# Optimization experiments

Measured on AMD Instinct MI355X. Metric: run time of the kernel, lower is better.

The kernel has to match this reference:

```python
import jax, jax.numpy as jnp
import numpy as np

B, C, S, H, W = 8, 64, 64, 128, 128
HID = 32           # max(C//2, 8)
STEPS, DT, OMEGA_MAX = 10, 0.3, 2.0
EPS = 1e-5


def _dw(x, k):
    # depthwise 3x3 conv, NCHW, kernel [C,1,3,3]
    return jax.lax.conv_general_dilated(
        x, k, (1, 1), 'SAME',
        dimension_numbers=('NCHW', 'OIHW', 'NCHW'),
        feature_group_count=x.shape[1])


def _pw(x, w, b=None):
    # pointwise (1x1) conv as einsum, w: [out,in]
    y = jnp.einsum('bihw,oi->bohw', x, w)
    return y if b is None else y + b[None, :, None, None]


def _lrelu(x):
    return jax.nn.leaky_relu(x, 0.2)


def setup_inputs() -> dict:
    key = jax.random.key(0)
    ks = jax.random.split(key, 16)
    d = {
        'force': jax.random.normal(ks[0], (B, C, H, W), jnp.float32),
        'style': jax.random.normal(ks[1], (1, S, 1, 1), jnp.float32),
        'illum_feat': jax.random.normal(ks[2], (B, C, H, W), jnp.float32),
        # HyperEncoder 1x1 convs
        'h_w1': 0.05 * jax.random.normal(ks[3], (HID, C + S), jnp.float32),
        'h_b1': jnp.zeros((HID,), jnp.float32),
        'h_w2': 0.05 * jax.random.normal(ks[4], (HID, HID), jnp.float32),
        'h_b2': jnp.zeros((HID,), jnp.float32),
        'h_w3': 0.05 * jax.random.normal(ks[5], (4 * C, HID), jnp.float32),
        'h_b3': jnp.zeros((4 * C,), jnp.float32),
        # OscillatorCell convs (no bias)
        'dw_k': 0.05 * jax.random.normal(ks[6], (C, 1, 3, 3), jnp.float32),
        'pw_w': 0.05 * jax.random.normal(ks[7], (C, C), jnp.float32),
        # refine: dw3x3 (+bias), pw, lrelu, pw
        'r_dw_k': 0.05 * jax.random.normal(ks[8], (C, 1, 3, 3), jnp.float32),
        'r_dw_b': jnp.zeros((C,), jnp.float32),
        'r_pw1_w': 0.05 * jax.random.normal(ks[9], (C, C), jnp.float32),
        'r_pw1_b': jnp.zeros((C,), jnp.float32),
        'r_pw2_w': 0.05 * jax.random.normal(ks[10], (C, C), jnp.float32),
        'r_pw2_b': jnp.zeros((C,), jnp.float32),
        'layer_scale': 0.01 * jnp.ones((1, C, 1, 1), jnp.float32),
    }
    return d


def reference(force, style, illum_feat,
              h_w1, h_b1, h_w2, h_b2, h_w3, h_b3,
              dw_k, pw_w,
              r_dw_k, r_dw_b, r_pw1_w, r_pw1_b, r_pw2_w, r_pw2_b,
              layer_scale):
    force = force + 0.2 * illum_feat
    b, c, h, w = force.shape

    # HyperEncoder
    style_map = jnp.broadcast_to(style, (b, style.shape[1], h, w))
    u = jnp.concatenate([force, style_map], axis=1)
    u = _lrelu(_pw(u, h_w1, h_b1))
    u = _lrelu(_pw(u, h_w2, h_b2))
    p = _pw(u, h_w3, h_b3)
    wch, zch, gch, bch = jnp.split(p, 4, axis=1)
    omega = jax.nn.sigmoid(wch) * OMEGA_MAX
    zeta = jax.nn.sigmoid(zch)
    gamma = jax.nn.sigmoid(gch) * 2.0
    beta = jnp.tanh(bch)

    # unrolled symplectic-Euler oscillator recurrence
    def step(carry, _):
        x, v = carry
        coupling = _dw(x, dw_k) + _pw(x, pw_w)
        accel = force + coupling - 2.0 * zeta * omega * v - omega ** 2 * x
        v = v + accel * DT
        x = x + v * DT
        return (x, v), None

    x0 = jnp.zeros_like(force)
    (x, v), _ = jax.lax.scan(step, (x0, x0), None, length=STEPS)

    # instance norm (no affine) + style modulation
    fx = force + x
    mu = fx.mean(axis=(2, 3), keepdims=True)
    var = fx.var(axis=(2, 3), keepdims=True)
    out = gamma * ((fx - mu) / jnp.sqrt(var + EPS)) + beta

    # refine branch with layer scale
    r = _dw(out, r_dw_k) + r_dw_b[None, :, None, None]
    r = _lrelu(_pw(r, r_pw1_w, r_pw1_b))
    r = _pw(r, r_pw2_w, r_pw2_b)
    out = out + layer_scale * r
    return (out, x, v)
```

## Files before the change

kernel.cpp:

```cpp
#include <hip/hip_runtime.h>
#include <hip/hip_fp16.h>

#define Hn 128
#define Wn 128
#define HWn 16384
#define Cn 64
#define Bn 8
#define NTOT (Bn*Cn*HWn)
#define NPIX (Bn*HWn)
#define DTc 0.3f
#define EPSc 1e-5f

__device__ __forceinline__ float sigm(float t){ return 1.0f/(1.0f+__expf(-t)); }

__global__ void fuseF0(const float4* __restrict__ force, const float4* __restrict__ illum,
                       __half* __restrict__ F, __half* __restrict__ XA, __half* __restrict__ V)
{
    int i = blockIdx.x * blockDim.x + threadIdx.x;
    float4 f = force[i], il = illum[i];
    float a0 = f.x + 0.2f*il.x, a1 = f.y + 0.2f*il.y;
    float a2 = f.z + 0.2f*il.z, a3 = f.w + 0.2f*il.w;
    uint2 pf, px, pv;
    __half2 h;
    h = __floats2half2_rn(a0, a1);            pf.x = *(unsigned int*)&h;
    h = __floats2half2_rn(a2, a3);            pf.y = *(unsigned int*)&h;
    h = __floats2half2_rn(0.09f*a0, 0.09f*a1); px.x = *(unsigned int*)&h;
    h = __floats2half2_rn(0.09f*a2, 0.09f*a3); px.y = *(unsigned int*)&h;
    h = __floats2half2_rn(0.3f*a0, 0.3f*a1);   pv.x = *(unsigned int*)&h;
    h = __floats2half2_rn(0.3f*a2, 0.3f*a3);   pv.y = *(unsigned int*)&h;
    *reinterpret_cast<uint2*>(F  + 4*(size_t)i) = pf;
    *reinterpret_cast<uint2*>(XA + 4*(size_t)i) = px;
    *reinterpret_cast<uint2*>(V  + 4*(size_t)i) = pv;
}

__global__ void prep(const float* __restrict__ style, const float* __restrict__ w1,
                     const float* __restrict__ b1, const float* __restrict__ pw,
                     const float* __restrict__ pw1, const float* __restrict__ pw2,
                     const float* __restrict__ w3, const float* __restrict__ b3,
                     float* __restrict__ w1T, float* __restrict__ c1,
                     float* __restrict__ pwT, float* __restrict__ pw1T,
                     float* __restrict__ pw2T,
                     __half2* __restrict__ w3abP, __half2* __restrict__ w3gbP,
                     __half2* __restrict__ b3abP, __half2* __restrict__ b3gbP)
{
    int t = threadIdx.x;
    if (t < 32) {
        float s = b1[t];
        for (int k = 0; k < 64; k++) s += w1[t*128 + 64 + k] * style[k];
        c1[t] = s;
    }
    for (int i = t; i < 2048; i += 256) { int c = i >> 5, j = i & 31; w1T[i] = w1[j*128 + c]; }
    for (int i = t; i < 4096; i += 256) {
        int c = i >> 6, k = i & 63;
        pwT[i]  = pw[k*64 + c];
        pw1T[i] = pw1[k*64 + c];
        pw2T[i] = pw2[k*64 + c];
    }
    for (int i = t; i < 2048; i += 256) {
        int j = i >> 5, k = i & 31;
        w3abP[i] = __floats2half2_rn(w3[j*32 + k],         w3[(64 + j)*32 + k]);
        w3gbP[i] = __floats2half2_rn(w3[(128 + j)*32 + k], w3[(192 + j)*32 + k]);
    }
    if (t < 64) {
        b3abP[t] = __floats2half2_rn(b3[t],       b3[64 + t]);
        b3gbP[t] = __floats2half2_rn(b3[128 + t], b3[192 + t]);
    }
}

__global__ void hyperM(const __half* __restrict__ F,
                       const float* __restrict__ w1T, const float* __restrict__ c1,
                       const float* __restrict__ w2, const float* __restrict__ b2,
                       const __half2* __restrict__ w3abP, const __half2* __restrict__ w3gbP,
                       const __half2* __restrict__ b3abP, const __half2* __restrict__ b3gbP,
                       __half2* __restrict__ AB, __half2* __restrict__ GB)
{
    int p = blockIdx.x * blockDim.x + threadIdx.x;
    int b  = p >> 14;
    int sp = p & (HWn - 1);
    int base = b * Cn * HWn + sp;

    float u1[32];
#pragma unroll
    for (int j = 0; j < 32; j++) u1[j] = c1[j];
#pragma unroll 4
    for (int c = 0; c < 64; c++) {
        float fc = __half2float(F[base + c*HWn]);
        const float* __restrict__ wr = w1T + c*32;
#pragma unroll
        for (int j = 0; j < 32; j++) u1[j] += wr[j] * fc;
    }
#pragma unroll
    for (int j = 0; j < 32; j++) { float v = u1[j]; u1[j] = v > 0.f ? v : 0.2f*v; }

    float u2[32];
#pragma unroll
    for (int i = 0; i < 32; i++) {
        float s = b2[i];
#pragma unroll
        for (int j = 0; j < 32; j++) s += w2[i*32 + j] * u1[j];
        u2[i] = s > 0.f ? s : 0.2f*s;
    }
    __half2 u2b[32];
#pragma unroll
    for (int i = 0; i < 32; i++) u2b[i] = __half2half2(__float2half(u2[i]));

#pragma unroll 2
    for (int j = 0; j < 64; j++) {
        __half2 aab = b3abP[j];
        __half2 agb = b3gbP[j];
        const __half2* __restrict__ wa = w3abP + j*32;
        const __half2* __restrict__ wg = w3gbP + j*32;
#pragma unroll
        for (int i = 0; i < 32; i++) {
            aab = __hfma2(wa[i], u2b[i], aab);
            agb = __hfma2(wg[i], u2b[i], agb);
        }
        float2 tab = __half22float2(aab);
        float om = 2.0f * sigm(tab.x);
        float ze = sigm(tab.y);
        AB[base + j*HWn] = __floats2half2_rn(2.0f * ze * om, om * om);
        float2 tgb = __half22float2(agb);
        GB[base + j*HWn] = __floats2half2_rn(2.0f * sigm(tgb.x), tanhf(tgb.y));
    }
}

template <bool LAST>
__global__ void osc_step(const __half* __restrict__ Xin, __half* __restrict__ Xout,
                         __half* __restrict__ V, const __half* __restrict__ F,
                         const __half2* __restrict__ AB,
                         const float* __restrict__ dwk, const float* __restrict__ pwT,
                         float* __restrict__ Xf, float* __restrict__ Vf)
{
    int wid  = blockIdx.x;
    int slot = wid >> 3;
    int pc   = ((wid & 7) << 6) + (slot >> 2);
    int c0   = (slot & 3) << 4;
    int p = (pc << 8) + threadIdx.x;
    int b  = p >> 14;
    int sp = p & (HWn - 1);
    int y = sp >> 7, x = sp & 127;
    int base = b * Cn * HWn + sp;

    float acc[16];
#pragma unroll
    for (int k = 0; k < 16; k++) acc[k] = 0.f;
#pragma unroll 4
    for (int c = 0; c < 64; c++) {
        float xc = __half2float(Xin[base + c*HWn]);
        const float* __restrict__ wr = pwT + c*64 + c0;
#pragma unroll
        for (int k = 0; k < 16; k++) acc[k] += wr[k] * xc;
    }

    int   yo[3] = { y > 0 ? -Wn : 0, 0, y < Hn-1 ? Wn : 0 };
    int   xo[3] = { x > 0 ? -1  : 0, 0, x < Wn-1 ? 1  : 0 };
    float my[3] = { y > 0 ? 1.f : 0.f, 1.f, y < Hn-1 ? 1.f : 0.f };
    float mx[3] = { x > 0 ? 1.f : 0.f, 1.f, x < Wn-1 ? 1.f : 0.f };
    float mm[9]; int oo[9];
#pragma unroll
    for (int dy = 0; dy < 3; dy++)
#pragma unroll
        for (int dx = 0; dx < 3; dx++) { mm[dy*3+dx] = my[dy]*mx[dx]; oo[dy*3+dx] = yo[dy]+xo[dx]; }

#pragma unroll
    for (int cc = 0; cc < 16; cc++) {
        int c = c0 + cc;
        int cb = base + c*HWn;
        float tv[9];
#pragma unroll
        for (int t = 0; t < 9; t++) tv[t] = __half2float(Xin[cb + oo[t]]);
        float dws = 0.f;
#pragma unroll
        for (int t = 0; t < 9; t++) dws += (dwk[c*9 + t] * mm[t]) * tv[t];
        float xc = tv[4];
        float2 ab = __half22float2(AB[cb]);
        float vv = __half2float(V[cb]);
        float accel = __half2float(F[cb]) + acc[cc] + dws - ab.x * vv - ab.y * xc;
        vv += accel * DTc;
        float xn = xc + vv * DTc;
        if constexpr (!LAST) {
            V[cb] = __float2half(vv);
            Xout[cb] = __float2half(xn);
        } else {
            Xf[cb] = xn;
            Vf[cb] = vv;
        }
    }
}

__global__ void inorm_stats(const __half* __restrict__ F, const float* __restrict__ X,
                            float* __restrict__ mu, float* __restrict__ rs)
{
    int bc = blockIdx.x;
    int base = bc * HWn;
    const __half2* __restrict__ F2 = (const __half2*)(F + base);
    const float4*  __restrict__ X4 = (const float4*)(X + base);
    float s = 0.f, s2 = 0.f;
    for (int i = threadIdx.x; i < HWn/4; i += blockDim.x) {
        float4 xv = X4[i];
        float2 f0 = __half22float2(F2[2*i]);
        float2 f1 = __half22float2(F2[2*i+1]);
        float v0 = f0.x + xv.x, v1 = f0.y + xv.y, v2 = f1.x + xv.z, v3 = f1.y + xv.w;
        s += (v0 + v1) + (v2 + v3);
        s2 += (v0*v0 + v1*v1) + (v2*v2 + v3*v3);
    }
#pragma unroll
    for (int o = 32; o > 0; o >>= 1) { s += __shfl_down(s, o); s2 += __shfl_down(s2, o); }
    __shared__ float sh[16];
    int w = threadIdx.x >> 6, l = threadIdx.x & 63;
    if (l == 0) { sh[w] = s; sh[8 + w] = s2; }
    __syncthreads();
    if (threadIdx.x == 0) {
        float S = 0.f, S2 = 0.f;
        for (int i = 0; i < 4; i++) { S += sh[i]; S2 += sh[8 + i]; }
        float m = S / (float)HWn;
        float var = S2 / (float)HWn - m*m;
        mu[bc] = m;
        rs[bc] = rsqrtf(var + EPSc);
    }
}

__global__ void modulate(const __half* __restrict__ F, const float4* __restrict__ X4,
                         const uint4* __restrict__ GBu, const float* __restrict__ mu,
                         const float* __restrict__ rs, __half* __restrict__ outp)
{
    int e4 = blockIdx.x * blockDim.x + threadIdx.x;
    int bc = e4 >> 12;
    float m = mu[bc], r = rs[bc];
    uint2 fu = *reinterpret_cast<const uint2*>(F + 4*(size_t)e4);
    float2 f0 = __half22float2(*(__half2*)&fu.x);
    float2 f1 = __half22float2(*(__half2*)&fu.y);
    float4 xv = X4[e4];
    uint4 gb = GBu[e4];
    float2 g0 = __half22float2(*(__half2*)&gb.x);
    float2 g1 = __half22float2(*(__half2*)&gb.y);
    float2 g2 = __half22float2(*(__half2*)&gb.z);
    float2 g3 = __half22float2(*(__half2*)&gb.w);
    float o0 = g0.x * ((f0.x + xv.x - m) * r) + g0.y;
    float o1 = g1.x * ((f0.y + xv.y - m) * r) + g1.y;
    float o2 = g2.x * ((f1.x + xv.z - m) * r) + g2.y;
    float o3 = g3.x * ((f1.y + xv.w - m) * r) + g3.y;
    __half2 h01 = __floats2half2_rn(o0, o1);
    __half2 h23 = __floats2half2_rn(o2, o3);
    uint2 pack; pack.x = *(unsigned int*)&h01; pack.y = *(unsigned int*)&h23;
    *reinterpret_cast<uint2*>(outp + 4*(size_t)e4) = pack;
}

__global__ __launch_bounds__(512)
void refine(const __half* __restrict__ outp,
            const float* __restrict__ rdwk, const float* __restrict__ rdwb,
            const float* __restrict__ pw1T, const float* __restrict__ pb1,
            const float* __restrict__ pw2T, const float* __restrict__ pb2,
            const float* __restrict__ ls, float* __restrict__ out)
{
    __shared__ unsigned int rv2_s[64][64];
    __shared__ unsigned int act2_s[64][64];
    __shared__ __half w1s[64][64];
    __shared__ __half w2s[64][64];
    __shared__ float  dwks[576];
    __shared__ __half2 pb1h[32], pb2h[32];
    __shared__ float  rdwbs[64], lss[64];
    int t = threadIdx.x;
    for (int i = t; i < 4096; i += 512) {
        w1s[i>>6][i&63] = __float2half(pw1T[i]);
        w2s[i>>6][i&63] = __float2half(pw2T[i]);
    }
    for (int i = t; i < 576; i += 512) dwks[i] = rdwk[i];
    if (t < 64) { rdwbs[t]=rdwb[t]; lss[t]=ls[t]; }
    if (t < 32) {
        pb1h[t] = __floats2half2_rn(pb1[2*t], pb1[2*t+1]);
        pb2h[t] = __floats2half2_rn(pb2[2*t], pb2[2*t+1]);
    }

    int l  = t & 63;
    int g  = t >> 6;
    int c0 = g << 3;
    int row = blockIdx.x;
    int b = row >> 7, y = row & 127;
    int base = b * Cn * HWn + y * Wn;
    int px0 = l << 1;

    int   yo[3] = { y > 0 ? -Wn : 0, 0, y < Hn-1 ? Wn : 0 };
    float my[3] = { y > 0 ? 1.f : 0.f, 1.f, y < Hn-1 ? 1.f : 0.f };
    float wl = l > 0  ? 1.f : 0.f;
    float wr = l < 63 ? 1.f : 0.f;
    int loff = l > 0 ? -1 : 0;
    __syncthreads();

#pragma unroll
    for (int cc = 0; cc < 8; cc++) {
        int c = c0 + cc;
        int cb = base + c*HWn + px0;
        float rv0 = rdwbs[c], rv1 = rdwbs[c];
#pragma unroll
        for (int r = 0; r < 3; r++) {
            const __half* __restrict__ rp = outp + cb + yo[r];
            unsigned int cu = *reinterpret_cast<const unsigned int*>(rp);
            float2 ct = __half22float2(*(__half2*)&cu);
            float lf = __half2float(rp[loff]);
            float rt = __half2float(rp[2]);
            float k0 = dwks[c*9 + r*3 + 0] * my[r];
            float k1 = dwks[c*9 + r*3 + 1] * my[r];
            float k2 = dwks[c*9 + r*3 + 2] * my[r];
            rv0 += k0*(wl*lf) + k1*ct.x + k2*ct.y;
            rv1 += k0*ct.x + k1*ct.y + k2*(wr*rt);
        }
        __half2 hv = __floats2half2_rn(rv0, rv1);
        rv2_s[c][l] = *(unsigned int*)&hv;
    }
    __syncthreads();

    __half2 accA[4], accB[4];
#pragma unroll
    for (int q = 0; q < 4; q++) { accA[q] = pb1h[(c0 >> 1) + q]; accB[q] = accA[q]; }
#pragma unroll 8
    for (int c = 0; c < 64; c++) {
        unsigned int rvu = rv2_s[c][l];
        __half2 rvp = *(__half2*)&rvu;
        __half2 r0 = __half2half2(__low2half(rvp));
        __half2 r1 = __half2half2(__high2half(rvp));
        uint4 wq = *reinterpret_cast<const uint4*>(&w1s[c][c0]);
        __half2 w01 = *(__half2*)&wq.x, w23 = *(__half2*)&wq.y;
        __half2 w45 = *(__half2*)&wq.z, w67 = *(__half2*)&wq.w;
        accA[0] = __hfma2(w01, r0, accA[0]); accB[0] = __hfma2(w01, r1, accB[0]);
        accA[1] = __hfma2(w23, r0, accA[1]); accB[1] = __hfma2(w23, r1, accB[1]);
        accA[2] = __hfma2(w45, r0, accA[2]); accB[2] = __hfma2(w45, r1, accB[2]);
        accA[3] = __hfma2(w67, r0, accA[3]); accB[3] = __hfma2(w67, r1, accB[3]);
    }
#pragma unroll
    for (int q = 0; q < 4; q++) {
        float2 a0 = __half22float2(accA[q]);
        float2 a1 = __half22float2(accB[q]);
        float e0 = a0.x > 0.f ? a0.x : 0.2f*a0.x;
        float e1 = a0.y > 0.f ? a0.y : 0.2f*a0.y;
        float e2 = a1.x > 0.f ? a1.x : 0.2f*a1.x;
        float e3 = a1.y > 0.f ? a1.y : 0.2f*a1.y;
        __half2 p0 = __floats2half2_rn(e0, e2);
        __half2 p1 = __floats2half2_rn(e1, e3);
        act2_s[c0 + 2*q][l]     = *(unsigned int*)&p0;
        act2_s[c0 + 2*q + 1][l] = *(unsigned int*)&p1;
    }
    __syncthreads();

#pragma unroll
    for (int q = 0; q < 4; q++) { accA[q] = pb2h[(c0 >> 1) + q]; accB[q] = accA[q]; }
#pragma unroll 8
    for (int j = 0; j < 64; j++) {
        unsigned int au = act2_s[j][l];
        __half2 ap = *(__half2*)&au;
        __half2 a0 = __half2half2(__low2half(ap));
        __half2 a1 = __half2half2(__high2half(ap));
        uint4 wq = *reinterpret_cast<const uint4*>(&w2s[j][c0]);
        __half2 w01 = *(__half2*)&wq.x, w23 = *(__half2*)&wq.y;
        __half2 w45 = *(__half2*)&wq.z, w67 = *(__half2*)&wq.w;
        accA[0] = __hfma2(w01, a0, accA[0]); accB[0] = __hfma2(w01, a1, accB[0]);
        accA[1] = __hfma2(w23, a0, accA[1]); accB[1] = __hfma2(w23, a1, accB[1]);
        accA[2] = __hfma2(w45, a0, accA[2]); accB[2] = __hfma2(w45, a1, accB[2]);
        accA[3] = __hfma2(w67, a0, accA[3]); accB[3] = __hfma2(w67, a1, accB[3]);
    }
#pragma unroll
    for (int q = 0; q < 4; q++) {
        float2 a0 = __half22float2(accA[q]);
        float2 a1 = __half22float2(accB[q]);
        int ca = c0 + 2*q, cb2 = ca + 1;
        int ba = base + ca*HWn + px0;
        int bb = base + cb2*HWn + px0;
        unsigned int oua = *reinterpret_cast<const unsigned int*>(outp + ba);
        unsigned int oub = *reinterpret_cast<const unsigned int*>(outp + bb);
        float2 oa = __half22float2(*(__half2*)&oua);
        float2 ob = __half22float2(*(__half2*)&oub);
        float la = lss[ca], lb = lss[cb2];
        *reinterpret_cast<float2*>(out + ba) = make_float2(oa.x + la*a0.x, oa.y + la*a1.x);
        *reinterpret_cast<float2*>(out + bb) = make_float2(ob.x + lb*a0.y, ob.y + lb*a1.y);
    }
}

extern "C" void kernel_launch(void* const* d_in, const int* in_sizes, int n_in,
                              void* d_out, int out_size, void* d_ws, size_t ws_size,
                              hipStream_t stream)
{
    (void)in_sizes; (void)n_in; (void)out_size; (void)ws_size;
    const float* force   = (const float*)d_in[0];
    const float* style   = (const float*)d_in[1];
    const float* illum   = (const float*)d_in[2];
    const float* h_w1    = (const float*)d_in[3];
    const float* h_b1    = (const float*)d_in[4];
    const float* h_w2    = (const float*)d_in[5];
    const float* h_b2    = (const float*)d_in[6];
    const float* h_w3    = (const float*)d_in[7];
    const float* h_b3    = (const float*)d_in[8];
    const float* dw_k    = (const float*)d_in[9];
    const float* pw_w    = (const float*)d_in[10];
    const float* r_dw_k  = (const float*)d_in[11];
    const float* r_dw_b  = (const float*)d_in[12];
    const float* r_pw1_w = (const float*)d_in[13];
    const float* r_pw1_b = (const float*)d_in[14];
    const float* r_pw2_w = (const float*)d_in[15];
    const float* r_pw2_b = (const float*)d_in[16];
    const float* lscale  = (const float*)d_in[17];

    float* out  = (float*)d_out;
    float* Xf32 = out + (size_t)NTOT;
    float* Vf32 = out + 2*(size_t)NTOT;
    __half2* GB = (__half2*)out;

    char* w = (char*)d_ws;
    __half2* AB = (__half2*)w; w += (size_t)NTOT*4;
    __half*  F  = (__half*)w;  w += (size_t)NTOT*2;
    __half*  XA = (__half*)w;  w += (size_t)NTOT*2;
    __half*  XB = (__half*)w;  w += (size_t)NTOT*2;
    __half*  Vh = (__half*)w;  w += (size_t)NTOT*2;
    float* w1T  = (float*)w;
    float* c1   = w1T + 2048;
    float* pwT  = c1 + 32;
    float* pw1T = pwT + 4096;
    float* pw2T = pw1T + 4096;
    float* mu   = pw2T + 4096;
    float* rs   = mu + 512;
    __half2* w3abP = (__half2*)(rs + 512);
    __half2* w3gbP = w3abP + 2048;
    __half2* b3abP = w3gbP + 2048;
    __half2* b3gbP = b3abP + 64;
    __half* outp = (__half*)AB;

    fuseF0<<<NTOT/1024, 256, 0, stream>>>((const float4*)force, (const float4*)illum,
                                          F, XA, Vh);
    prep<<<1, 256, 0, stream>>>(style, h_w1, h_b1, pw_w, r_pw1_w, r_pw2_w, h_w3, h_b3,
                                w1T, c1, pwT, pw1T, pw2T, w3abP, w3gbP, b3abP, b3gbP);
    hyperM<<<NPIX/256, 256, 0, stream>>>(F, w1T, c1, h_w2, h_b2,
                                         w3abP, w3gbP, b3abP, b3gbP, AB, GB);
    for (int s = 1; s <= 8; s++) {
        const __half* xin = (s & 1) ? XA : XB;
        __half*      xout = (s & 1) ? XB : XA;
        osc_step<false><<<2048, 256, 0, stream>>>(xin, xout, Vh, F, AB,
                                                  dw_k, pwT, nullptr, nullptr);
    }
    osc_step<true><<<2048, 256, 0, stream>>>(XA, XB, Vh, F, AB,
                                             dw_k, pwT, Xf32, Vf32);
    inorm_stats<<<Bn*Cn, 256, 0, stream>>>(F, Xf32, mu, rs);
    modulate<<<NTOT/1024, 256, 0, stream>>>(F, (const float4*)Xf32,
                                            (const uint4*)GB, mu, rs, outp);
    refine<<<NPIX/128, 512, 0, stream>>>(outp, r_dw_k, r_dw_b, pw1T, r_pw1_b,
                                         pw2T, r_pw2_b, lscale, out);
}
```

Measured before the change: 495.1 us.

## Stage oscillator stencil and hyper inputs in LDS, split hyper output heads

Each osc_step block now handles one half-row across all 64 channels. It stages the three input rows plus halo in shared memory, so the pointwise and 3x3 depthwise reads come from LDS instead of repeated global gathers. The hyper encoder loads its F tile into shared memory with vector loads. It also splits the AB and GB output heads across a second grid dimension, which adds parallelism but recomputes the first two layers twice. The trade-off is extra LDS traffic, a block-level sync, and duplicated hyper MLP work.

After: 911.9 us. +84.2%, slower.

```diff
diff --git a/kernel.cpp b/kernel.cpp
--- a/kernel.cpp
+++ b/kernel.cpp
@@ -67,24 +67,38 @@
     }
 }
 
-__global__ void hyperM(const __half* __restrict__ F,
-                       const float* __restrict__ w1T, const float* __restrict__ c1,
-                       const float* __restrict__ w2, const float* __restrict__ b2,
-                       const __half2* __restrict__ w3abP, const __half2* __restrict__ w3gbP,
-                       const __half2* __restrict__ b3abP, const __half2* __restrict__ b3gbP,
-                       __half2* __restrict__ AB, __half2* __restrict__ GB)
-{
-    int p = blockIdx.x * blockDim.x + threadIdx.x;
-    int b  = p >> 14;
-    int sp = p & (HWn - 1);
-    int base = b * Cn * HWn + sp;
+__global__ __launch_bounds__(256)
+void hyperS(const __half* __restrict__ F,
+            const float* __restrict__ w1T, const float* __restrict__ c1,
+            const float* __restrict__ w2, const float* __restrict__ b2,
+            const __half2* __restrict__ w3abP, const __half2* __restrict__ w3gbP,
+            const __half2* __restrict__ b3abP, const __half2* __restrict__ b3gbP,
+            __half2* __restrict__ AB, __half2* __restrict__ GB)
+{
+    __shared__ __half fs[64][256];
+    int t = threadIdx.x;
+    int p0 = blockIdx.x << 8;
+    int b  = p0 >> 14;
+    int sp0 = p0 & (HWn - 1);
+    int tbase = b * Cn * HWn + sp0;
+
+#pragma unroll
+    for (int it = 0; it < 8; it++) {
+        int f = t + (it << 8);
+        int c = f >> 5, u = f & 31;
+        uint4 d = *reinterpret_cast<const uint4*>(F + tbase + c*HWn + (u << 3));
+        *reinterpret_cast<uint4*>(&fs[c][u << 3]) = d;
+    }
+    __syncthreads();
+
+    int base = tbase + t;
 
     float u1[32];
 #pragma unroll
     for (int j = 0; j < 32; j++) u1[j] = c1[j];
 #pragma unroll 4
     for (int c = 0; c < 64; c++) {
-        float fc = __half2float(F[base + c*HWn]);
+        float fc = __half2float(fs[c][t]);
         const float* __restrict__ wr = w1T + c*32;
 #pragma unroll
         for (int j = 0; j < 32; j++) u1[j] += wr[j] * fc;
@@ -104,75 +118,104 @@
 #pragma unroll
     for (int i = 0; i < 32; i++) u2b[i] = __half2half2(__float2half(u2[i]));
 
+    if (blockIdx.y == 0) {
 #pragma unroll 2
-    for (int j = 0; j < 64; j++) {
-        __half2 aab = b3abP[j];
-        __half2 agb = b3gbP[j];
-        const __half2* __restrict__ wa = w3abP + j*32;
-        const __half2* __restrict__ wg = w3gbP + j*32;
-#pragma unroll
-        for (int i = 0; i < 32; i++) {
-            aab = __hfma2(wa[i], u2b[i], aab);
-            agb = __hfma2(wg[i], u2b[i], agb);
+        for (int j = 0; j < 64; j++) {
+            __half2 aab = b3abP[j];
+            const __half2* __restrict__ wa = w3abP + j*32;
+#pragma unroll
+            for (int i = 0; i < 32; i++) aab = __hfma2(wa[i], u2b[i], aab);
+            float2 tab = __half22float2(aab);
+            float om = 2.0f * sigm(tab.x);
+            float ze = sigm(tab.y);
+            AB[base + j*HWn] = __floats2half2_rn(2.0f * ze * om, om * om);
         }
-        float2 tab = __half22float2(aab);
-        float om = 2.0f * sigm(tab.x);
-        float ze = sigm(tab.y);
-        AB[base + j*HWn] = __floats2half2_rn(2.0f * ze * om, om * om);
-        float2 tgb = __half22float2(agb);
-        GB[base + j*HWn] = __floats2half2_rn(2.0f * sigm(tgb.x), tanhf(tgb.y));
+    } else {
+#pragma unroll 2
+        for (int j = 0; j < 64; j++) {
+            __half2 agb = b3gbP[j];
+            const __half2* __restrict__ wg = w3gbP + j*32;
+#pragma unroll
+            for (int i = 0; i < 32; i++) agb = __hfma2(wg[i], u2b[i], agb);
+            float2 tgb = __half22float2(agb);
+            GB[base + j*HWn] = __floats2half2_rn(2.0f * sigm(tgb.x), tanhf(tgb.y));
+        }
     }
 }
 
 template <bool LAST>
-__global__ void osc_step(const __half* __restrict__ Xin, __half* __restrict__ Xout,
-                         __half* __restrict__ V, const __half* __restrict__ F,
-                         const __half2* __restrict__ AB,
-                         const float* __restrict__ dwk, const float* __restrict__ pwT,
-                         float* __restrict__ Xf, float* __restrict__ Vf)
-{
-    int wid  = blockIdx.x;
-    int slot = wid >> 3;
-    int pc   = ((wid & 7) << 6) + (slot >> 2);
-    int c0   = (slot & 3) << 4;
-    int p = (pc << 8) + threadIdx.x;
-    int b  = p >> 14;
-    int sp = p & (HWn - 1);
-    int y = sp >> 7, x = sp & 127;
-    int base = b * Cn * HWn + sp;
+__global__ __launch_bounds__(256)
+void osc_step(const __half* __restrict__ Xin, __half* __restrict__ Xout,
+              __half* __restrict__ V, const __half* __restrict__ F,
+              const __half2* __restrict__ AB,
+              const float* __restrict__ dwk, const float* __restrict__ pwT,
+              float* __restrict__ Xf, float* __restrict__ Vf)
+{
+    __shared__ __half xs[64][3][68];
+    int wid = blockIdx.x;
+    int hp  = ((wid & 7) << 8) + (wid >> 3);
+    int b   = hp >> 8;
+    int hr  = hp & 255;
+    int y   = hr >> 1;
+    int xh  = (hr & 1) << 6;
+    int t   = threadIdx.x;
+    int base0 = b * Cn * HWn + y * Wn + xh;
+
+    int   yo[3] = { y > 0 ? -Wn : 0, 0, y < Hn-1 ? Wn : 0 };
+    float my[3] = { y > 0 ? 1.f : 0.f, 1.f, y < Hn-1 ? 1.f : 0.f };
+
+#pragma unroll
+    for (int it = 0; it < 24; it++) {
+        int f = t + (it << 8);
+        int c = f / 96;
+        int rem = f - c*96;
+        int r = rem >> 5;
+        int u = rem & 31;
+        unsigned int d = *reinterpret_cast<const unsigned int*>(Xin + base0 + c*HWn + yo[r] + (u << 1));
+        *reinterpret_cast<unsigned int*>(&xs[c][r][2 + (u << 1)]) = d;
+    }
+    for (int hv = t; hv < 384; hv += 256) {
+        int c = hv / 6;
+        int rem = hv - c*6;
+        int r = rem >> 1;
+        int side = rem & 1;
+        xs[c][r][side ? 66 : 1] = Xin[base0 + c*HWn + yo[r] + (side ? 64 : -1)];
+    }
+    __syncthreads();
+
+    int l  = t & 63;
+    int c0 = (t >> 6) << 4;
+    int x  = xh + l;
+    float wl = x > 0      ? 1.f : 0.f;
+    float wr = x < Wn - 1 ? 1.f : 0.f;
 
     float acc[16];
 #pragma unroll
     for (int k = 0; k < 16; k++) acc[k] = 0.f;
 #pragma unroll 4
     for (int c = 0; c < 64; c++) {
-        float xc = __half2float(Xin[base + c*HWn]);
-        const float* __restrict__ wr = pwT + c*64 + c0;
-#pragma unroll
-        for (int k = 0; k < 16; k++) acc[k] += wr[k] * xc;
-    }
-
-    int   yo[3] = { y > 0 ? -Wn : 0, 0, y < Hn-1 ? Wn : 0 };
-    int   xo[3] = { x > 0 ? -1  : 0, 0, x < Wn-1 ? 1  : 0 };
-    float my[3] = { y > 0 ? 1.f : 0.f, 1.f, y < Hn-1 ? 1.f : 0.f };
-    float mx[3] = { x > 0 ? 1.f : 0.f, 1.f, x < Wn-1 ? 1.f : 0.f };
-    float mm[9]; int oo[9];
-#pragma unroll
-    for (int dy = 0; dy < 3; dy++)
-#pragma unroll
-        for (int dx = 0; dx < 3; dx++) { mm[dy*3+dx] = my[dy]*mx[dx]; oo[dy*3+dx] = yo[dy]+xo[dx]; }
+        float xc = __half2float(xs[c][1][2 + l]);
+        const float* __restrict__ wrow = pwT + c*64 + c0;
+#pragma unroll
+        for (int k = 0; k < 16; k++) acc[k] += wrow[k] * xc;
+    }
 
 #pragma unroll
     for (int cc = 0; cc < 16; cc++) {
         int c = c0 + cc;
-        int cb = base + c*HWn;
-        float tv[9];
-#pragma unroll
-        for (int t = 0; t < 9; t++) tv[t] = __half2float(Xin[cb + oo[t]]);
+        int cb = base0 + l + c*HWn;
         float dws = 0.f;
 #pragma unroll
-        for (int t = 0; t < 9; t++) dws += (dwk[c*9 + t] * mm[t]) * tv[t];
-        float xc = tv[4];
+        for (int r = 0; r < 3; r++) {
+            float lf = __half2float(xs[c][r][1 + l]);
+            float ct = __half2float(xs[c][r][2 + l]);
+            float rt = __half2float(xs[c][r][3 + l]);
+            float k0 = dwk[c*9 + r*3 + 0] * my[r];
+            float k1 = dwk[c*9 + r*3 + 1] * my[r];
+            float k2 = dwk[c*9 + r*3 + 2] * my[r];
+            dws += k0 * (wl * lf) + k1 * ct + k2 * (wr * rt);
+        }
+        float xc = __half2float(xs[c][1][2 + l]);
         float2 ab = __half22float2(AB[cb]);
         float vv = __half2float(V[cb]);
         float accel = __half2float(F[cb]) + acc[cc] + dws - ab.x * vv - ab.y * xc;
@@ -427,8 +470,8 @@
                                           F, XA, Vh);
     prep<<<1, 256, 0, stream>>>(style, h_w1, h_b1, pw_w, r_pw1_w, r_pw2_w, h_w3, h_b3,
                                 w1T, c1, pwT, pw1T, pw2T, w3abP, w3gbP, b3abP, b3gbP);
-    hyperM<<<NPIX/256, 256, 0, stream>>>(F, w1T, c1, h_w2, h_b2,
-                                         w3abP, w3gbP, b3abP, b3gbP, AB, GB);
+    hyperS<<<dim3(NPIX/256, 2), 256, 0, stream>>>(F, w1T, c1, h_w2, h_b2,
+                                                  w3abP, w3gbP, b3abP, b3gbP, AB, GB);
     for (int s = 1; s <= 8; s++) {
         const __half* xin = (s & 1) ? XA : XB;
         __half*      xout = (s & 1) ? XB : XA;
```

## Split hyper-encoder into hidden-layer kernel and two-way output-head kernel

Applied to the files above, without the earlier changes.

The fused hyper-encoder kernel is split in two. The first computes the two hidden layers per pixel, staging F through shared memory with vectorized loads, and writes a 32-half hidden vector per pixel into scratch space borrowed from the X output buffer. The second reads that vector and uses a 2-wide grid in y, so the omega/zeta head and the gamma/beta head run in separate blocks. The aim is more parallelism and lower register pressure per thread, at the cost of an extra round trip through global memory for the intermediate and one more launch.

Result: faster. 482.4 us (-2.6%).

```diff
diff --git a/kernel.cpp b/kernel.cpp
--- a/kernel.cpp
+++ b/kernel.cpp
@@ -67,60 +67,109 @@
     }
 }
 
-__global__ void hyperM(const __half* __restrict__ F,
-                       const float* __restrict__ w1T, const float* __restrict__ c1,
-                       const float* __restrict__ w2, const float* __restrict__ b2,
-                       const __half2* __restrict__ w3abP, const __half2* __restrict__ w3gbP,
-                       const __half2* __restrict__ b3abP, const __half2* __restrict__ b3gbP,
-                       __half2* __restrict__ AB, __half2* __restrict__ GB)
+__global__ __launch_bounds__(256)
+void hyperU(const __half* __restrict__ F,
+            const float* __restrict__ w1T, const float* __restrict__ c1,
+            const float* __restrict__ w2, const float* __restrict__ b2,
+            __half* __restrict__ U2)
+{
+    __shared__ __half fs[64][256];
+    int t = threadIdx.x;
+    int p0 = blockIdx.x << 8;
+    int b  = p0 >> 14;
+    int sp0 = p0 & (HWn - 1);
+    int tbase = b * Cn * HWn + sp0;
+
+#pragma unroll
+    for (int it = 0; it < 8; it++) {
+        int f = t + (it << 8);
+        int c = f >> 5, u = f & 31;
+        uint4 d = *reinterpret_cast<const uint4*>(F + tbase + c*HWn + (u << 3));
+        *reinterpret_cast<uint4*>(&fs[c][u << 3]) = d;
+    }
+    __syncthreads();
+
+    float u1[32];
+#pragma unroll
+    for (int j = 0; j < 32; j++) u1[j] = c1[j];
+#pragma unroll 4
+    for (int c = 0; c < 64; c++) {
+        float fc = __half2float(fs[c][t]);
+        const float* __restrict__ wr = w1T + c*32;
+#pragma unroll
+        for (int j = 0; j < 32; j++) u1[j] += wr[j] * fc;
+    }
+#pragma unroll
+    for (int j = 0; j < 32; j++) { float v = u1[j]; u1[j] = v > 0.f ? v : 0.2f*v; }
+
+    float u2[32];
+#pragma unroll
+    for (int i = 0; i < 32; i++) {
+        float s = b2[i];
+#pragma unroll
+        for (int j = 0; j < 32; j++) s += w2[i*32 + j] * u1[j];
+        u2[i] = s > 0.f ? s : 0.2f*s;
+    }
+
+    uint4* dst = reinterpret_cast<uint4*>(U2 + ((size_t)(p0 + t)) * 32);
+#pragma unroll
+    for (int q = 0; q < 4; q++) {
+        __half2 h0 = __floats2half2_rn(u2[8*q+0], u2[8*q+1]);
+        __half2 h1 = __floats2half2_rn(u2[8*q+2], u2[8*q+3]);
+        __half2 h2 = __floats2half2_rn(u2[8*q+4], u2[8*q+5]);
+        __half2 h3 = __floats2half2_rn(u2[8*q+6], u2[8*q+7]);
+        uint4 d;
+        d.x = *(unsigned int*)&h0; d.y = *(unsigned int*)&h1;
+        d.z = *(unsigned int*)&h2; d.w = *(unsigned int*)&h3;
+        dst[q] = d;
+    }
+}
+
+__global__ __launch_bounds__(256)
+void hyperW(const __half* __restrict__ U2,
+            const __half2* __restrict__ w3abP, const __half2* __restrict__ w3gbP,
+            const __half2* __restrict__ b3abP, const __half2* __restrict__ b3gbP,
+            __half2* __restrict__ AB, __half2* __restrict__ GB)
 {
     int p = blockIdx.x * blockDim.x + threadIdx.x;
     int b  = p >> 14;
     int sp = p & (HWn - 1);
     int base = b * Cn * HWn + sp;
 
-    float u1[32];
-#pragma unroll
-    for (int j = 0; j < 32; j++) u1[j] = c1[j];
-#pragma unroll 4
-    for (int c = 0; c < 64; c++) {
-        float fc = __half2float(F[base + c*HWn]);
-        const float* __restrict__ wr = w1T + c*32;
-#pragma unroll
-        for (int j = 0; j < 32; j++) u1[j] += wr[j] * fc;
-    }
-#pragma unroll
-    for (int j = 0; j < 32; j++) { float v = u1[j]; u1[j] = v > 0.f ? v : 0.2f*v; }
-
-    float u2[32];
-#pragma unroll
-    for (int i = 0; i < 32; i++) {
-        float s = b2[i];
-#pragma unroll
-        for (int j = 0; j < 32; j++) s += w2[i*32 + j] * u1[j];
-        u2[i] = s > 0.f ? s : 0.2f*s;
-    }
     __half2 u2b[32];
-#pragma unroll
-    for (int i = 0; i < 32; i++) u2b[i] = __half2half2(__float2half(u2[i]));
-
+    const uint4* src = reinterpret_cast<const uint4*>(U2 + (size_t)p * 32);
+#pragma unroll
+    for (int q = 0; q < 4; q++) {
+        uint4 d = src[q];
+        __half2 h;
+        h = *(__half2*)&d.x; u2b[8*q+0] = __half2half2(__low2half(h)); u2b[8*q+1] = __half2half2(__high2half(h));
+        h = *(__half2*)&d.y; u2b[8*q+2] = __half2half2(__low2half(h)); u2b[8*q+3] = __half2half2(__high2half(h));
+        h = *(__half2*)&d.z; u2b[8*q+4] = __half2half2(__low2half(h)); u2b[8*q+5] = __half2half2(__high2half(h));
+        h = *(__half2*)&d.w; u2b[8*q+6] = __half2half2(__low2half(h)); u2b[8*q+7] = __half2half2(__high2half(h));
+    }
+
+    if (blockIdx.y == 0) {
 #pragma unroll 2
-    for (int j = 0; j < 64; j++) {
-        __half2 aab = b3abP[j];
-        __half2 agb = b3gbP[j];
-        const __half2* __restrict__ wa = w3abP + j*32;
-        const __half2* __restrict__ wg = w3gbP + j*32;
-#pragma unroll
-        for (int i = 0; i < 32; i++) {
-            aab = __hfma2(wa[i], u2b[i], aab);
-            agb = __hfma2(wg[i], u2b[i], agb);
+        for (int j = 0; j < 64; j++) {
+            __half2 aab = b3abP[j];
+            const __half2* __restrict__ wa = w3abP + j*32;
+#pragma unroll
+            for (int i = 0; i < 32; i++) aab = __hfma2(wa[i], u2b[i], aab);
+            float2 tab = __half22float2(aab);
+            float om = 2.0f * sigm(tab.x);
+            float ze = sigm(tab.y);
+            AB[base + j*HWn] = __floats2half2_rn(2.0f * ze * om, om * om);
         }
-        float2 tab = __half22float2(aab);
-        float om = 2.0f * sigm(tab.x);
-        float ze = sigm(tab.y);
-        AB[base + j*HWn] = __floats2half2_rn(2.0f * ze * om, om * om);
-        float2 tgb = __half22float2(agb);
-        GB[base + j*HWn] = __floats2half2_rn(2.0f * sigm(tgb.x), tanhf(tgb.y));
+    } else {
+#pragma unroll 2
+        for (int j = 0; j < 64; j++) {
+            __half2 agb = b3gbP[j];
+            const __half2* __restrict__ wg = w3gbP + j*32;
+#pragma unroll
+            for (int i = 0; i < 32; i++) agb = __hfma2(wg[i], u2b[i], agb);
+            float2 tgb = __half22float2(agb);
+            GB[base + j*HWn] = __floats2half2_rn(2.0f * sigm(tgb.x), tanhf(tgb.y));
+        }
     }
 }
 
@@ -403,6 +452,7 @@
     float* Xf32 = out + (size_t)NTOT;
     float* Vf32 = out + 2*(size_t)NTOT;
     __half2* GB = (__half2*)out;
+    __half*  U2h = (__half*)Xf32;
 
     char* w = (char*)d_ws;
     __half2* AB = (__half2*)w; w += (size_t)NTOT*4;
@@ -427,8 +477,8 @@
                                           F, XA, Vh);
     prep<<<1, 256, 0, stream>>>(style, h_w1, h_b1, pw_w, r_pw1_w, r_pw2_w, h_w3, h_b3,
                                 w1T, c1, pwT, pw1T, pw2T, w3abP, w3gbP, b3abP, b3gbP);
-    hyperM<<<NPIX/256, 256, 0, stream>>>(F, w1T, c1, h_w2, h_b2,
-                                         w3abP, w3gbP, b3abP, b3gbP, AB, GB);
+    hyperU<<<NPIX/256, 256, 0, stream>>>(F, w1T, c1, h_w2, h_b2, U2h);
+    hyperW<<<dim3(NPIX/256, 2), 256, 0, stream>>>(U2h, w3abP, w3gbP, b3abP, b3gbP, AB, GB);
     for (int s = 1; s <= 8; s++) {
         const __half* xin = (s & 1) ? XA : XB;
         __half*      xout = (s & 1) ? XB : XA;
```
